# Optimization experiments

Hardware: AMD Instinct MI355X
Metric: run time of the kernel (lower is better)

The kernel has to match this reference:

```python
import jax, jax.numpy as jnp
from jax import lax
import numpy as np

MAX_D = 4  # max_displacement


def conv3x3(x, w, b):
    # x: [B,Cin,H,W], w: [Cout,Cin,3,3], SAME padding (pad=1)
    y = lax.conv_general_dilated(
        x, w, window_strides=(1, 1), padding='SAME',
        dimension_numbers=('NCHW', 'OIHW', 'NCHW'))
    return y + b[None, :, None, None]


def compute_cost_volume(f1, f2, d):
    # roll+mask in the torch code == shift with zero padding:
    # cv[idx,h,w] = mean_c f1[c,h,w] * f2[c,h-i,w-j] (zero outside bounds)
    B, C, H, W = f1.shape
    pad = jnp.pad(f2, ((0, 0), (0, 0), (d, d), (d, d)))
    slices = []
    for i in range(-d, d + 1):
        for j in range(-d, d + 1):
            shifted = lax.dynamic_slice(pad, (0, 0, d - i, d - j), (B, C, H, W))
            slices.append((f1 * shifted).sum(axis=1) / C)  # [B,H,W]
    return jnp.stack(slices, axis=1)  # [B,81,H,W]


def setup_inputs() -> dict:
    key = jax.random.key(0)
    ks = jax.random.split(key, 10)
    B, C, H, W = 16, 64, 128, 128
    cv_ch = (2 * MAX_D + 1) ** 2  # 81
    def w_init(k, shape):
        fan_in = shape[1] * shape[2] * shape[3]
        return jax.random.normal(k, shape, dtype=jnp.float32) * np.float32(np.sqrt(2.0 / fan_in))
    return {
        'f1': jax.random.normal(ks[0], (B, C, H, W), dtype=jnp.float32),
        'f2_warped': jax.random.normal(ks[1], (B, C, H, W), dtype=jnp.float32),
        'w1': w_init(ks[2], (128, C + cv_ch, 3, 3)),
        'b1': jnp.zeros((128,), dtype=jnp.float32),
        'w2': w_init(ks[3], (64, 128, 3, 3)),
        'b2': jnp.zeros((64,), dtype=jnp.float32),
        'w3': w_init(ks[4], (32, 64, 3, 3)),
        'b3': jnp.zeros((32,), dtype=jnp.float32),
        'w4': w_init(ks[5], (2, 32, 3, 3)),
        'b4': jnp.zeros((2,), dtype=jnp.float32),
    }


def reference(f1, f2_warped, w1, b1, w2, b2, w3, b3, w4, b4):
    cv = compute_cost_volume(f1, f2_warped, MAX_D)       # [B,81,H,W]
    x = jnp.concatenate([f1, cv], axis=1)                # [B,145,H,W]
    x = jax.nn.relu(conv3x3(x, w1, b1))
    x = jax.nn.relu(conv3x3(x, w2, b2))
    x = jax.nn.relu(conv3x3(x, w3, b3))
    flow = conv3x3(x, w4, b4)                            # [B,2,H,W]
    return flow
```

## Files before the change

### kernel.cpp

```cpp
#include <hip/hip_runtime.h>


typedef __bf16 bf16x8 __attribute__((ext_vector_type(8)));
typedef float f32x4 __attribute__((ext_vector_type(4)));

__device__ __forceinline__ unsigned short f2bf_bits(float f) {
  unsigned int u = __float_as_uint(f);
  unsigned int r = (u + 0x7FFFu + ((u >> 16) & 1u)) >> 16;
  return (unsigned short)r;
}

__device__ __forceinline__ void glds16(const ushort* gp, ushort* lp) {
  __builtin_amdgcn_global_load_lds((const __attribute__((address_space(1))) void*)gp,
                                   (__attribute__((address_space(3))) void*)lp, 16, 0, 0);
}

__global__ void prep_w_kernel(const float* __restrict__ w, uint4* __restrict__ wp,
                              int CIN, int COUT, int CHUNKS, int NFRAG) {
  int idx = blockIdx.x * 256 + threadIdx.x;
  int total = CHUNKS * 9 * NFRAG * 64;
  if (idx >= total) return;
  int lane = idx & 63;
  int fi = idx >> 6;
  int nf = fi % NFRAG;
  int t = fi / NFRAG;
  int rs = t % 9;
  int c = t / 9;
  int co = nf * 16 + (lane & 15);
  int cib = c * 32 + (lane >> 4) * 8;
  union { uint4 q; ushort s[8]; } pk;
#pragma unroll
  for (int e = 0; e < 8; ++e) {
    int ci = cib + e;
    float v = (ci < CIN && co < COUT) ? w[(co * CIN + ci) * 9 + rs] : 0.f;
    pk.s[e] = f2bf_bits(v);
  }
  wp[idx] = pk.q;
}

__global__ __launch_bounds__(256) void pack_f1_kernel(const float* __restrict__ f1,
                                                      ushort* __restrict__ xf1) {
  __shared__ float tile[64][132];
  const int bid = blockIdx.x;
  const int h = bid & 127, b = bid >> 7;
  const int tid = threadIdx.x;
  for (int e = tid; e < 64 * 128; e += 256) {
    int c = e >> 7, w = e & 127;
    tile[c][w] = f1[((b * 64 + c) * 128 + h) * 128 + w];
  }
  __syncthreads();
  const int px = tid >> 1, cgb = (tid & 1) * 4;
  const long base = ((long)(b * 128 + h) * 128 + px) * 64;
#pragma unroll
  for (int e = 0; e < 4; ++e) {
    int c0 = (cgb + e) * 8;
    union { uint4 q; ushort s[8]; } pk;
#pragma unroll
    for (int k = 0; k < 8; ++k) pk.s[k] = f2bf_bits(tile[c0 + k][px]);
    *reinterpret_cast<uint4*>(&xf1[base + c0]) = pk.q;
  }
}

__global__ __launch_bounds__(256)
void cost_volume_mfma_kernel(const ushort* __restrict__ xf1,
                             const ushort* __restrict__ xf2,
                             ushort* __restrict__ xcv) {
  const int bx = blockIdx.x;
  const int idx = bx >> 3;
  const int b = 2 * (bx & 7) + (idx >> 7);
  const int h = idx & 127;
  const int tid = threadIdx.x;
  const int lane = tid & 63;
  const int g = tid >> 6;
  const int l15 = lane & 15;
  const int lg = lane >> 4;

  __shared__ __align__(16) float sC[4][2][16][33];
  __shared__ __align__(16) ushort sO[96][132];

  {
    uint4 z = make_uint4(0u, 0u, 0u, 0u);
    uint4* p = (uint4*)sO;
#pragma unroll
    for (int j = 0; j < 7; ++j) {
      int e = tid + j * 256;
      if (e < 1584) p[e] = z;
    }
  }
  __syncthreads();

  const int w0g = g * 32;
  bf16x8 afr[2][2];
  {
    const ushort* f1p = xf1 + ((long)(b * 128 + h) * 128) * 64;
#pragma unroll
    for (int wt = 0; wt < 2; ++wt)
#pragma unroll
      for (int kc = 0; kc < 2; ++kc) {
        int pix = w0g + wt * 16 + l15;
        afr[wt][kc] = *reinterpret_cast<const bf16x8*>(f1p + pix * 64 + kc * 32 + lg * 8);
      }
  }

  const float inv = 1.0f / 64.0f;
  for (int A = 0; A < 9; ++A) {
    int fr = h - 4 + A;
    if ((unsigned)fr >= 128u) continue;
    const ushort* f2p = xf2 + ((long)(b * 128 + fr) * 128) * 64;
    bf16x8 bfr[3][2];
#pragma unroll
    for (int t = 0; t < 3; ++t)
#pragma unroll
      for (int kc = 0; kc < 2; ++kc) {
        int p = w0g - 4 + t * 16 + l15;
        uint4 v = make_uint4(0u, 0u, 0u, 0u);
        if ((unsigned)p < 128u)
          v = *reinterpret_cast<const uint4*>(f2p + (long)p * 64 + kc * 32 + lg * 8);
        bfr[t][kc] = __builtin_bit_cast(bf16x8, v);
      }
#pragma unroll
    for (int wt = 0; wt < 2; ++wt)
#pragma unroll
      for (int nt = 0; nt < 2; ++nt) {
        f32x4 acc = {0.f, 0.f, 0.f, 0.f};
        acc = __builtin_amdgcn_mfma_f32_16x16x32_bf16(afr[wt][0], bfr[wt + nt][0], acc, 0, 0, 0);
        acc = __builtin_amdgcn_mfma_f32_16x16x32_bf16(afr[wt][1], bfr[wt + nt][1], acc, 0, 0, 0);
#pragma unroll
        for (int j = 0; j < 4; ++j)
          sC[g][wt][lg * 4 + j][nt * 16 + l15] = acc[j];
      }
    const int chb = (8 - A) * 9;
#pragma unroll
    for (int wt = 0; wt < 2; ++wt) {
      int px = w0g + wt * 16 + l15;
#pragma unroll
      for (int u = 0; u < 3; ++u) {
        if (u < ((lg == 3) ? 3 : 2)) {
          int tj = lg * 2 + u;
          float v = sC[g][wt][l15][l15 + 8 - tj];
          sO[chb + tj][px] = f2bf_bits(v * inv);
        }
      }
    }
  }
  __syncthreads();

  uint4* dst = reinterpret_cast<uint4*>(xcv + ((long)(b * 128 + h) * 128) * 96);
#pragma unroll
  for (int j = 0; j < 6; ++j) {
    int t8 = j * 256 + tid;
    int px = t8 / 12;
    int ch0 = (t8 - px * 12) * 8;
    union { uint4 qq; ushort ss[8]; } pk;
#pragma unroll
    for (int k = 0; k < 8; ++k) pk.ss[k] = sO[ch0 + k][px];
    dst[t8] = pk.qq;
  }
}

template <int CA, int CB, int COUT, bool RELU, bool PLANAR>
__global__ __launch_bounds__(512, 2)
void conv_mfma_kernel(const ushort* __restrict__ xa, const ushort* __restrict__ xb,
                      const uint4* __restrict__ wp, const float* __restrict__ bias,
                      void* __restrict__ outv) {
  constexpr int CHUNKS = (CA + CB) / 32;
  constexpr int NFRAG = COUT / 16;
  constexpr int NFW = (NFRAG >= 2) ? NFRAG / 2 : 1;
  constexpr int MFW = (NFRAG >= 2) ? 4 : 2;
  constexpr int SXN = 4 * 130 * 32;
  constexpr int WTQ = 9 * NFRAG * 64;
  constexpr int WI = (WTQ + 511) / 512;
  constexpr int SO_STRIDE = COUT + 4;
  constexpr int STAGE_B = PLANAR ? 2048 : 2 * 128 * SO_STRIDE * 2;
  constexpr int SX_B = 2 * SXN * 2;
  constexpr int BASE_B = SX_B + WTQ * 16;
  constexpr int ARENA_B = STAGE_B > BASE_B ? STAGE_B : BASE_B;

  __shared__ __align__(16) char arena[ARENA_B];
  ushort* sXa = (ushort*)arena;
  ushort* sWt = (ushort*)(arena + SX_B);

  const int bx = blockIdx.x;
  const int idx = bx >> 3;
  const int b = 2 * (bx & 7) + (idx >> 6);
  const int h0 = (idx & 63) * 2;
  const int tid = threadIdx.x;
  const int lane = tid & 63;
  const int wid = tid >> 6;
  const int l15 = lane & 15;
  const int lg = lane >> 4;
  const int cg    = (NFRAG >= 2) ? (wid >> 2) : 0;
  const int row   = (NFRAG >= 2) ? ((wid >> 1) & 1) : (wid >> 2);
  const int pbase = (NFRAG >= 2) ? ((wid & 1) * 64) : ((wid & 3) * 32);

  f32x4 acc[MFW][NFW];
#pragma unroll
  for (int mf = 0; mf < MFW; ++mf)
#pragma unroll
    for (int nf = 0; nf < NFW; ++nf) acc[mf][nf] = {0.f, 0.f, 0.f, 0.f};

  if (tid < 64) {
    int bi = tid >> 5, tr = (tid >> 3) & 3, wz = (tid >> 2) & 1, gq = tid & 3;
    int wl = wz ? 129 : 0;
    *reinterpret_cast<uint4*>(&sXa[bi * SXN + ((tr * 130 + wl) * 4 + gq) * 8]) =
        make_uint4(0u, 0u, 0u, 0u);
  }
  if (h0 == 0 || h0 == 126) {
    const int trz = (h0 == 0) ? 0 : 3;
#pragma unroll
    for (int e = 0; e < 2; ++e) {
      int u = tid + e * 512;
      int bi = u >> 9, k = u & 511;
      *reinterpret_cast<uint4*>(&sXa[bi * SXN + ((trz * 130 + 1) * 4 + k) * 8]) =
          make_uint4(0u, 0u, 0u, 0u);
    }
  }

  auto stage = [&](int c, int bi) {
    const int c0 = c * 32;
    const ushort* src;
    int cst, coff;
    if (CB == 0 || c0 < CA) { src = xa; cst = CA; coff = c0; }
    else                    { src = xb; cst = CB; coff = c0 - CA; }
    const int tr = wid >> 1;
    const int gh = h0 - 1 + tr;
    if ((unsigned)gh < 128u) {
      const ushort* rowp = src + ((long)(b * 128 + gh) * 128) * cst + coff;
#pragma unroll
      for (int t = 0; t < 4; ++t) {
        int s = (wid & 1) * 4 + t;
        int u = s * 64 + lane;
        int wl = 1 + (u >> 2);
        int gq = lane & 3;
        int sw = (wl + (wl >> 2)) & 3;
        const ushort* gp = rowp + (long)(wl - 1) * cst + (gq ^ sw) * 8;
        ushort* lp = &sXa[bi * SXN + ((tr * 130 + 1) * 4 + s * 64) * 8];
        glds16(gp, lp);
      }
    }
  };

  auto stage_wt = [&](int c) {
    const ushort* src = (const ushort*)(wp + (size_t)c * WTQ);
#pragma unroll
    for (int i = 0; i < WI; ++i) {
      int e = tid + i * 512;
      if ((WTQ & 511) == 0 || e < WTQ)
        glds16(src + e * 8, sWt + (size_t)(tid & ~63) * 8 + (size_t)(i * 512) * 8);
    }
  };

  stage(0, 0);
  stage_wt(0);
  __syncthreads();

  for (int c = 0; c < CHUNKS; ++c) {
    if (c + 1 < CHUNKS) stage(c + 1, (c + 1) & 1);
    const int bi = c & 1;
#pragma unroll
    for (int rs = 0; rs < 9; ++rs) {
      const int r = rs / 3, s = rs % 3;
      const int tr = row + r;
      bf16x8 afr[MFW];
#pragma unroll
      for (int mf = 0; mf < MFW; ++mf) {
        int wl = pbase + mf * 16 + l15 + s;
        int sw = (wl + (wl >> 2)) & 3;
        afr[mf] = *reinterpret_cast<const bf16x8*>(
            &sXa[bi * SXN + ((tr * 130 + wl) * 4 + (lg ^ sw)) * 8]);
      }
      const ushort* wrow = sWt + (size_t)(rs * NFRAG + cg * NFW) * 64 * 8;
#pragma unroll
      for (int nf = 0; nf < NFW; ++nf) {
        bf16x8 bfr = *reinterpret_cast<const bf16x8*>(wrow + (nf * 64 + lane) * 8);
#pragma unroll
        for (int mf = 0; mf < MFW; ++mf)
          acc[mf][nf] = __builtin_amdgcn_mfma_f32_16x16x32_bf16(afr[mf], bfr, acc[mf][nf], 0, 0, 0);
      }
    }
    __syncthreads();
    if (c + 1 < CHUNKS) stage_wt(c + 1);
    __syncthreads();
  }

  if (!PLANAR) {
    ushort* sO = (ushort*)arena;
#pragma unroll
    for (int nf = 0; nf < NFW; ++nf) {
      float bs = bias[cg * NFW * 16 + nf * 16 + l15];
#pragma unroll
      for (int mf = 0; mf < MFW; ++mf) {
        int px2 = row * 128 + pbase + mf * 16 + lg * 4;
#pragma unroll
        for (int j = 0; j < 4; ++j) {
          float v = acc[mf][nf][j] + bs;
          if (RELU) v = fmaxf(v, 0.f);
          sO[(px2 + j) * SO_STRIDE + cg * NFW * 16 + nf * 16 + l15] = f2bf_bits(v);
        }
      }
    }
    __syncthreads();
    constexpr int QPP = COUT / 8;
    uint4* dst = reinterpret_cast<uint4*>((ushort*)outv + ((long)(b * 128 + h0) * 128) * COUT);
#pragma unroll
    for (int t0 = 0; t0 < 2 * 128 * QPP / 512; ++t0) {
      int t = t0 * 512 + tid;
      int px2 = t / QPP;
      int ch0 = (t & (QPP - 1)) * 8;
      union { uint4 qq; ushort ss[8]; } pk;
#pragma unroll
      for (int k = 0; k < 8; ++k) pk.ss[k] = sO[px2 * SO_STRIDE + ch0 + k];
      dst[t] = pk.qq;
    }
  } else {
    float* sF = (float*)arena;
    if (l15 < 2) {
#pragma unroll
      for (int mf = 0; mf < MFW; ++mf) {
        int pxb = pbase + mf * 16 + lg * 4;
#pragma unroll
        for (int j = 0; j < 4; ++j)
          sF[(l15 * 2 + row) * 128 + pxb + j] = acc[mf][0][j] + bias[l15];
      }
    }
    __syncthreads();
    float* out = (float*)outv;
    if (tid < 128) {
      int ch = tid >> 6, r = (tid >> 5) & 1, qx = tid & 31;
      *reinterpret_cast<float4*>(&out[((long)(b * 2 + ch) * 128 + h0 + r) * 128 + qx * 4]) =
          *reinterpret_cast<float4*>(&sF[(ch * 2 + r) * 128 + qx * 4]);
    }
  }
}

extern "C" void kernel_launch(void* const* d_in, const int* in_sizes, int n_in,
                              void* d_out, int out_size, void* d_ws, size_t ws_size,
                              hipStream_t stream) {
  (void)in_sizes; (void)n_in; (void)out_size; (void)ws_size;
  const float* f1 = (const float*)d_in[0];
  const float* f2 = (const float*)d_in[1];
  const float* w1 = (const float*)d_in[2];
  const float* b1 = (const float*)d_in[3];
  const float* w2 = (const float*)d_in[4];
  const float* b2 = (const float*)d_in[5];
  const float* w3 = (const float*)d_in[6];
  const float* b3 = (const float*)d_in[7];
  const float* w4 = (const float*)d_in[8];
  const float* b4 = (const float*)d_in[9];

  char* ws = (char*)d_ws;
  size_t off = 0;
  ushort* xf1 = (ushort*)(ws + off); off += (size_t)262144 * 64 * 2;
  ushort* xcv = (ushort*)(ws + off); off += (size_t)262144 * 96 * 2;
  ushort* x1  = (ushort*)(ws + off); off += (size_t)262144 * 128 * 2;
  ushort* x2  = (ushort*)(ws + off); off += (size_t)262144 * 64 * 2;
  uint4* wp1 = (uint4*)(ws + off); off += (size_t)5 * 9 * 8 * 64 * 16;
  uint4* wp2 = (uint4*)(ws + off); off += (size_t)4 * 9 * 4 * 64 * 16;
  uint4* wp3 = (uint4*)(ws + off); off += (size_t)2 * 9 * 2 * 64 * 16;
  uint4* wp4 = (uint4*)(ws + off); off += (size_t)1 * 9 * 1 * 64 * 16;
  ushort* x3  = xf1;
  ushort* xf2 = x1;

  prep_w_kernel<<<90, 256, 0, stream>>>(w1, wp1, 145, 128, 5, 8);
  prep_w_kernel<<<36, 256, 0, stream>>>(w2, wp2, 128, 64, 4, 4);
  prep_w_kernel<<<9, 256, 0, stream>>>(w3, wp3, 64, 32, 2, 2);
  prep_w_kernel<<<3, 256, 0, stream>>>(w4, wp4, 32, 2, 1, 1);

  pack_f1_kernel<<<2048, 256, 0, stream>>>(f1, xf1);
  pack_f1_kernel<<<2048, 256, 0, stream>>>(f2, xf2);
  cost_volume_mfma_kernel<<<2048, 256, 0, stream>>>(xf1, xf2, xcv);

  conv_mfma_kernel<64, 96, 128, true, false><<<1024, 512, 0, stream>>>(xf1, xcv, wp1, b1, x1);
  conv_mfma_kernel<128, 0, 64, true, false><<<1024, 512, 0, stream>>>(x1, x1, wp2, b2, x2);
  conv_mfma_kernel<64, 0, 32, true, false><<<1024, 512, 0, stream>>>(x2, x2, wp3, b3, x3);
  conv_mfma_kernel<32, 0, 16, false, true><<<1024, 512, 0, stream>>>(x3, x3, wp4, b4, d_out);
}
```

Before: 322.2 us.

## Split weight staging into two halves to overlap weight loads with MFMA compute

Splits each chunk's 9 filter taps into two LDS weight buffers (5 taps and 4 taps). The second half's weights load while the first half computes, and the next chunk's first half loads while the second half computes. This hides the weight-load latency that was previously exposed between the two barriers. LDS size stays the same, but the extra lambda structure may raise register pressure, and there is a possible race because the glds writes are not waited on before the barrier.

Result: faster. 309.0 us (-4.1%).

```diff
diff --git a/kernel.cpp b/kernel.cpp
--- a/kernel.cpp
+++ b/kernel.cpp
@@ -169,16 +169,20 @@
   constexpr int MFW = (NFRAG >= 2) ? 4 : 2;
   constexpr int SXN = 4 * 130 * 32;
   constexpr int WTQ = 9 * NFRAG * 64;
-  constexpr int WI = (WTQ + 511) / 512;
+  constexpr int WTA_Q = 5 * NFRAG * 64;
+  constexpr int WTB_Q = 4 * NFRAG * 64;
+  constexpr int WIA = (WTA_Q + 511) / 512;
+  constexpr int WIB = (WTB_Q + 511) / 512;
   constexpr int SO_STRIDE = COUT + 4;
   constexpr int STAGE_B = PLANAR ? 2048 : 2 * 128 * SO_STRIDE * 2;
   constexpr int SX_B = 2 * SXN * 2;
-  constexpr int BASE_B = SX_B + WTQ * 16;
+  constexpr int BASE_B = SX_B + (WTA_Q + WTB_Q) * 16;
   constexpr int ARENA_B = STAGE_B > BASE_B ? STAGE_B : BASE_B;
 
   __shared__ __align__(16) char arena[ARENA_B];
   ushort* sXa = (ushort*)arena;
-  ushort* sWt = (ushort*)(arena + SX_B);
+  ushort* sWtA = (ushort*)(arena + SX_B);
+  ushort* sWtB = (ushort*)(arena + SX_B + WTA_Q * 16);
 
   const int bx = blockIdx.x;
   const int idx = bx >> 3;
@@ -240,25 +244,28 @@
     }
   };
 
-  auto stage_wt = [&](int c) {
+  auto stage_wtA = [&](int c) {
     const ushort* src = (const ushort*)(wp + (size_t)c * WTQ);
 #pragma unroll
-    for (int i = 0; i < WI; ++i) {
+    for (int i = 0; i < WIA; ++i) {
       int e = tid + i * 512;
-      if ((WTQ & 511) == 0 || e < WTQ)
-        glds16(src + e * 8, sWt + (size_t)(tid & ~63) * 8 + (size_t)(i * 512) * 8);
+      if ((WTA_Q % 512) == 0 || e < WTA_Q)
+        glds16(src + (size_t)e * 8, sWtA + (size_t)(tid & ~63) * 8 + (size_t)(i * 512) * 8);
     }
   };
-
-  stage(0, 0);
-  stage_wt(0);
-  __syncthreads();
-
-  for (int c = 0; c < CHUNKS; ++c) {
-    if (c + 1 < CHUNKS) stage(c + 1, (c + 1) & 1);
-    const int bi = c & 1;
-#pragma unroll
-    for (int rs = 0; rs < 9; ++rs) {
+  auto stage_wtB = [&](int c) {
+    const ushort* src = (const ushort*)(wp + (size_t)c * WTQ + WTA_Q);
+#pragma unroll
+    for (int i = 0; i < WIB; ++i) {
+      int e = tid + i * 512;
+      if ((WTB_Q % 512) == 0 || e < WTB_Q)
+        glds16(src + (size_t)e * 8, sWtB + (size_t)(tid & ~63) * 8 + (size_t)(i * 512) * 8);
+    }
+  };
+
+  auto compute = [&](int bi, int rs0, int rs1, const ushort* wbuf) {
+#pragma unroll
+    for (int rs = rs0; rs < rs1; ++rs) {
       const int r = rs / 3, s = rs % 3;
       const int tr = row + r;
       bf16x8 afr[MFW];
@@ -269,7 +276,7 @@
         afr[mf] = *reinterpret_cast<const bf16x8*>(
             &sXa[bi * SXN + ((tr * 130 + wl) * 4 + (lg ^ sw)) * 8]);
       }
-      const ushort* wrow = sWt + (size_t)(rs * NFRAG + cg * NFW) * 64 * 8;
+      const ushort* wrow = wbuf + (size_t)((rs - rs0) * NFRAG + cg * NFW) * 64 * 8;
 #pragma unroll
       for (int nf = 0; nf < NFW; ++nf) {
         bf16x8 bfr = *reinterpret_cast<const bf16x8*>(wrow + (nf * 64 + lane) * 8);
@@ -278,8 +285,20 @@
           acc[mf][nf] = __builtin_amdgcn_mfma_f32_16x16x32_bf16(afr[mf], bfr, acc[mf][nf], 0, 0, 0);
       }
     }
+  };
+
+  stage(0, 0);
+  stage_wtA(0);
+  __syncthreads();
+
+  for (int c = 0; c < CHUNKS; ++c) {
+    const int bi = c & 1;
+    if (c + 1 < CHUNKS) stage(c + 1, (c + 1) & 1);
+    stage_wtB(c);
+    compute(bi, 0, 5, sWtA);
     __syncthreads();
-    if (c + 1 < CHUNKS) stage_wt(c + 1);
+    if (c + 1 < CHUNKS) stage_wtA(c + 1);
+    compute(bi, 5, 9, sWtB);
     __syncthreads();
   }
 
```
